# Optimization experiments

Hardware: AMD Instinct MI355X
Metric: run time of the kernel (lower is better)

Reference implementation:

```python
import jax, jax.numpy as jnp
import numpy as np

D_MODEL = 1024
NUM_HEADS = 16
DEPTH = D_MODEL // NUM_HEADS
B, S = 4, 2048


def setup_inputs() -> dict:
    key = jax.random.key(0)
    ks = jax.random.split(key, 13)
    sd = 1.0 / np.sqrt(D_MODEL)
    inp = {
        "q_in": jax.random.normal(ks[0], (B, S, D_MODEL), jnp.float32),
        "k_in": jax.random.normal(ks[1], (B, S, D_MODEL), jnp.float32),
        "v_in": jax.random.normal(ks[2], (B, S, D_MODEL), jnp.float32),
        # binary padding/causal-style mask: 1 = masked position
        "m_in": (jax.random.uniform(ks[3], (B, 1, S, S)) < 0.1).astype(jnp.float32),
        "Wq": jax.random.normal(ks[4], (D_MODEL, D_MODEL), jnp.float32) * sd,
        "bq": jax.random.normal(ks[5], (D_MODEL,), jnp.float32) * 0.01,
        "Wk": jax.random.normal(ks[6], (D_MODEL, D_MODEL), jnp.float32) * sd,
        "bk": jax.random.normal(ks[7], (D_MODEL,), jnp.float32) * 0.01,
        "Wv": jax.random.normal(ks[8], (D_MODEL, D_MODEL), jnp.float32) * sd,
        "bv": jax.random.normal(ks[9], (D_MODEL,), jnp.float32) * 0.01,
        "Wo": jax.random.normal(ks[10], (D_MODEL, D_MODEL), jnp.float32) * sd,
        "bo": jax.random.normal(ks[11], (D_MODEL,), jnp.float32) * 0.01,
    }
    return inp


def _split(t):
    # [B,S,D] -> [B,H,S,depth]
    b, s, _ = t.shape
    return t.reshape(b, s, NUM_HEADS, DEPTH).transpose(0, 2, 1, 3)


def reference(q_in, k_in, v_in, m_in, Wq, bq, Wk, bk, Wv, bv, Wo, bo):
    # torch Linear: x @ W^T + b
    q = _split(q_in @ Wq.T + bq)
    k = _split(k_in @ Wk.T + bk)
    v = _split(v_in @ Wv.T + bv)
    scale = jnp.sqrt(jnp.asarray(DEPTH, jnp.float32))
    scores = jnp.einsum("bhqd,bhkd->bhqk", q, k) / scale
    scores = scores - m_in * 1e6
    attn = jax.nn.softmax(scores, axis=-1)
    out = jnp.einsum("bhqk,bhkd->bhqd", attn, v)  # [B,H,S,depth]
    out = out.transpose(0, 2, 1, 3).reshape(q_in.shape[0], -1, D_MODEL)
    return out @ Wo.T + bo
```

## Files before the change

### kernel.cpp

```cpp
#include <hip/hip_runtime.h>


typedef __bf16 bf16_t;
typedef __bf16 bf16x4 __attribute__((ext_vector_type(4)));
typedef __bf16 bf16x8 __attribute__((ext_vector_type(8)));
typedef float floatx4 __attribute__((ext_vector_type(4)));
typedef float floatx16 __attribute__((ext_vector_type(16)));

#define DMODEL 1024
#define NHEAD  16
#define DEPTH  64
#define BATCH  4
#define SEQ    2048
#define MROWS  (BATCH * SEQ)

#define QSCALE 0.18033688011112042f

#define GLDS16(gaddr, laddr)                                                   \
  __builtin_amdgcn_global_load_lds(                                            \
      (__attribute__((address_space(1))) void*)(gaddr),                        \
      (__attribute__((address_space(3))) void*)(laddr), 16, 0, 0)

__global__ __launch_bounds__(256) void cvt_weights(
    const float* __restrict__ w0, const float* __restrict__ w1,
    const float* __restrict__ w2, const float* __restrict__ w3,
    bf16_t* __restrict__ out) {
  const int n_per4 = (DMODEL * DMODEL) / 4;
  int idx = blockIdx.x * blockDim.x + threadIdx.x;
  int t = idx / n_per4;
  int e4 = idx - t * n_per4;
  const float* src = (t == 0) ? w0 : (t == 1) ? w1 : (t == 2) ? w2 : w3;
  const float sc = (t == 0) ? QSCALE : 1.0f;
  float4 v = ((const float4*)src)[e4];
  bf16_t* dst = out + (size_t)t * (DMODEL * DMODEL) + (size_t)e4 * 4;
  dst[0] = (bf16_t)(v.x * sc); dst[1] = (bf16_t)(v.y * sc);
  dst[2] = (bf16_t)(v.z * sc); dst[3] = (bf16_t)(v.w * sc);
}

__global__ __launch_bounds__(256) void cvt3(
    const float* __restrict__ q, const float* __restrict__ k,
    const float* __restrict__ v, bf16_t* __restrict__ dst) {
  const size_t n8 = (size_t)MROWS * DMODEL / 8;
  size_t i = (size_t)blockIdx.x * blockDim.x + threadIdx.x;
  int t = (int)(i / n8);
  size_t e = i - (size_t)t * n8;
  const float* src = (t == 0) ? q : (t == 1) ? k : v;
  const float4* s = (const float4*)(src + e * 8);
  float4 f0 = s[0], f1 = s[1];
  bf16x8 o;
  o[0] = (bf16_t)f0.x; o[1] = (bf16_t)f0.y; o[2] = (bf16_t)f0.z; o[3] = (bf16_t)f0.w;
  o[4] = (bf16_t)f1.x; o[5] = (bf16_t)f1.y; o[6] = (bf16_t)f1.z; o[7] = (bf16_t)f1.w;
  *(bf16x8*)(dst + i * 8) = o;
}

__global__ __launch_bounds__(256) void mask_prepack(
    const float* __restrict__ m, unsigned int* __restrict__ M32) {
  size_t t = (size_t)blockIdx.x * blockDim.x + threadIdx.x;
  int lane = (int)(t & 63);
  int it = (int)((t >> 6) & 31);
  int g  = (int)((t >> 11) & 63);
  int b  = (int)(t >> 17);
  int q  = g * 32 + (lane & 31);
  int hi = lane >> 5;
  const float* row = m + ((size_t)b * SEQ + q) * SEQ + it * 64;
  unsigned int bits = 0;
#pragma unroll
  for (int kb = 0; kb < 2; kb++) {
#pragma unroll
    for (int rc = 0; rc < 4; rc++) {
      const int base = kb * 32 + 16 * (rc >> 1) + 8 * hi + 4 * (rc & 1);
      const float4 mv = *(const float4*)(row + base);
      const int bit0 = kb * 16 + rc * 4;
      if (mv.x == 0.f) bits |= 1u << (bit0 + 0);
      if (mv.y == 0.f) bits |= 1u << (bit0 + 1);
      if (mv.z == 0.f) bits |= 1u << (bit0 + 2);
      if (mv.w == 0.f) bits |= 1u << (bit0 + 3);
    }
  }
  M32[t] = bits;
}

__global__ __launch_bounds__(256) void gemm_qkv(
    const bf16_t* __restrict__ Abf3, const bf16_t* __restrict__ Wbf,
    const float* __restrict__ bq, const float* __restrict__ bk,
    const float* __restrict__ bv, bf16_t* __restrict__ Qh,
    bf16_t* __restrict__ Kh, bf16_t* __restrict__ Vth) {
  __shared__ __align__(16) bf16_t As[128 * 32];
  __shared__ __align__(16) bf16_t Bs[128 * 32];
  const int K = DMODEL;
  const int tid = threadIdx.x;
  const int lane = tid & 63;
  const int w = tid >> 6;
  const int quad = lane >> 4;
  const int l16 = lane & 15;
  const int wm = w & 1, wn = w >> 1;
  const int z = blockIdx.z;

  const bf16_t* A = Abf3 + (size_t)z * MROWS * DMODEL;
  const bf16_t* Bt = Wbf + (size_t)z * DMODEL * DMODEL;
  const float* bias = (z == 0) ? bq : (z == 1) ? bk : bv;
  const float bias_scale = (z == 0) ? QSCALE : 1.0f;
  bf16_t* Ov = (z == 0) ? Qh : (z == 1) ? Kh : Vth;

  const int lin = blockIdx.x + 8 * blockIdx.y;
  const int c = lin & 7;
  const int j = lin >> 3;
  const int n0 = (j & 7) * 128;
  const int m0 = ((j >> 3) * 8 + c) * 128;

  const int r4 = lane >> 2;
  const int c4 = (lane & 3) ^ (r4 & 3);
  const bf16_t* Ag = A + (size_t)(m0 + w * 32 + r4) * K + c4 * 8;
  const bf16_t* Bg = Bt + (size_t)(n0 + w * 32 + r4) * K + c4 * 8;
  char* AsB = (char*)As + (w * 32) * 64;
  char* BsB = (char*)Bs + (w * 32) * 64;

  floatx4 acc[4][4] = {};

  for (int kk = 0; kk < K; kk += 32) {
    __syncthreads();
    GLDS16(Ag + kk, AsB);
    GLDS16(Ag + kk + (size_t)16 * K, AsB + 16 * 64);
    GLDS16(Bg + kk, BsB);
    GLDS16(Bg + kk + (size_t)16 * K, BsB + 16 * 64);
    __syncthreads();

    bf16x8 af[4], bfr[4];
#pragma unroll
    for (int mi = 0; mi < 4; mi++) {
      const char* Arow = (const char*)As + (wm * 64 + mi * 16 + l16) * 64;
      af[mi] = *(const bf16x8*)(Arow + ((quad ^ (l16 & 3)) * 16));
    }
#pragma unroll
    for (int ni = 0; ni < 4; ni++) {
      const char* Brow = (const char*)Bs + (wn * 64 + ni * 16 + l16) * 64;
      bfr[ni] = *(const bf16x8*)(Brow + ((quad ^ (l16 & 3)) * 16));
    }
#pragma unroll
    for (int mi = 0; mi < 4; mi++)
#pragma unroll
      for (int ni = 0; ni < 4; ni++)
        acc[mi][ni] = __builtin_amdgcn_mfma_f32_16x16x32_bf16(af[mi], bfr[ni], acc[mi][ni], 0, 0, 0);
  }

#pragma unroll
  for (int ni = 0; ni < 4; ni++) {
    const int col = n0 + wn * 64 + ni * 16 + l16;
    const float bvl = bias_scale * bias[col];
    const int hh = col >> 6, d = col & (DEPTH - 1);
#pragma unroll
    for (int mi = 0; mi < 4; mi++) {
#pragma unroll
      for (int r = 0; r < 4; r++) {
        const int row = m0 + wm * 64 + mi * 16 + quad * 4 + r;
        const float val = acc[mi][ni][r] + bvl;
        const int bb = row >> 11, s = row & (SEQ - 1);
        if (z != 2) {
          Ov[((((size_t)bb * NHEAD + hh) * SEQ + s) << 6) + d] = (bf16_t)val;
        } else {
          Ov[(((size_t)bb * NHEAD + hh) * DEPTH + d) * SEQ + s] = (bf16_t)val;
        }
      }
    }
  }
}

__global__ __launch_bounds__(256) void gemm_wo(
    const bf16_t* __restrict__ A, const bf16_t* __restrict__ Bt,
    const float* __restrict__ bias, float* __restrict__ Ov,
    int M, int N, int K) {
  __shared__ __align__(16) bf16_t As[128 * 32];
  __shared__ __align__(16) bf16_t Bs[128 * 32];
  const int tid = threadIdx.x;
  const int lane = tid & 63;
  const int w = tid >> 6;
  const int quad = lane >> 4;
  const int l16 = lane & 15;
  const int wm = w & 1, wn = w >> 1;

  const int lin = blockIdx.x + 8 * blockIdx.y;
  const int c = lin & 7;
  const int j = lin >> 3;
  const int n0 = (j & 7) * 128;
  const int m0 = ((j >> 3) * 8 + c) * 128;

  const int r4 = lane >> 2;
  const int c4 = (lane & 3) ^ (r4 & 3);
  const bf16_t* Ag = A + (size_t)(m0 + w * 32 + r4) * K + c4 * 8;
  const bf16_t* Bg = Bt + (size_t)(n0 + w * 32 + r4) * K + c4 * 8;
  char* AsB = (char*)As + (w * 32) * 64;
  char* BsB = (char*)Bs + (w * 32) * 64;

  floatx4 acc[4][4] = {};

  for (int kk = 0; kk < K; kk += 32) {
    __syncthreads();
    GLDS16(Ag + kk, AsB);
    GLDS16(Ag + kk + (size_t)16 * K, AsB + 16 * 64);
    GLDS16(Bg + kk, BsB);
    GLDS16(Bg + kk + (size_t)16 * K, BsB + 16 * 64);
    __syncthreads();

    bf16x8 af[4], bfr[4];
#pragma unroll
    for (int mi = 0; mi < 4; mi++) {
      const char* Arow = (const char*)As + (wm * 64 + mi * 16 + l16) * 64;
      af[mi] = *(const bf16x8*)(Arow + ((quad ^ (l16 & 3)) * 16));
    }
#pragma unroll
    for (int ni = 0; ni < 4; ni++) {
      const char* Brow = (const char*)Bs + (wn * 64 + ni * 16 + l16) * 64;
      bfr[ni] = *(const bf16x8*)(Brow + ((quad ^ (l16 & 3)) * 16));
    }
#pragma unroll
    for (int mi = 0; mi < 4; mi++)
#pragma unroll
      for (int ni = 0; ni < 4; ni++)
        acc[mi][ni] = __builtin_amdgcn_mfma_f32_16x16x32_bf16(af[mi], bfr[ni], acc[mi][ni], 0, 0, 0);
  }

#pragma unroll
  for (int ni = 0; ni < 4; ni++) {
    const int col = n0 + wn * 64 + ni * 16 + l16;
    const float bv = bias[col];
#pragma unroll
    for (int mi = 0; mi < 4; mi++)
#pragma unroll
      for (int r = 0; r < 4; r++) {
        const int row = m0 + wm * 64 + mi * 16 + quad * 4 + r;
        Ov[(size_t)row * N + col] = acc[mi][ni][r] + bv;
      }
  }
}

__global__ __launch_bounds__(256, 4) void attn_kernel(
    const bf16_t* __restrict__ Qh, const bf16_t* __restrict__ Kh,
    const bf16_t* __restrict__ Vt, const unsigned int* __restrict__ M32,
    bf16_t* __restrict__ O) {
  const int lane = threadIdx.x & 63;
  const int w = __builtin_amdgcn_readfirstlane(threadIdx.x >> 6);
  const int l31 = lane & 31;
  const int hi = lane >> 5;

  const int lin = blockIdx.x + 16 * blockIdx.y + 256 * blockIdx.z;
  const int x8 = lin & 7;
  const int kk = lin >> 3;
  const int qt = kk & 15;
  const int bh = ((kk >> 4) << 3) | x8;
  const int h = bh & 15;
  const int b = bh >> 4;
  const int q0 = qt * 128;

  const bf16_t* Qb = Qh + ((size_t)b * NHEAD + h) * SEQ * DEPTH;
  const bf16_t* Kb = Kh + ((size_t)b * NHEAD + h) * SEQ * DEPTH;
  const bf16_t* Vb = Vt + ((size_t)b * NHEAD + h) * DEPTH * SEQ;
  const unsigned int* Mw =
      M32 + ((size_t)b * 64 + (qt * 4 + w)) * 32 * 64 + lane;

  __shared__ __align__(16) bf16_t Ksm[64 * 64];
  __shared__ __align__(16) bf16_t Vsm[64 * 64];
  __shared__ float Lsm[4][32];

  const int r8 = lane >> 3;
  const int c8 = (lane & 7) ^ r8;
  const int i1 = w * 16 + r8;
  const int i2 = i1 + 8;
  const int lo1 = i1 & 31, lo2 = i2 & 31;
  const int s1 = (i1 & 32) | ((lo1 & ~12) | ((lo1 & 4) << 1) | ((lo1 & 8) >> 1));
  const int s2 = (i2 & 32) | ((lo2 & ~12) | ((lo2 & 4) << 1) | ((lo2 & 8) >> 1));
  const bf16_t* Kg1 = Kb + (size_t)s1 * DEPTH + c8 * 8;
  const bf16_t* Kg2 = Kb + (size_t)s2 * DEPTH + c8 * 8;
  const bf16_t* Vg  = Vb + (size_t)(w * 16 + r8) * SEQ + c8 * 8;
  const int woff = (w * 16) * 128;

  bf16x8 aq[4];
  {
    const bf16_t* qp = Qb + (size_t)(q0 + w * 32 + l31) * DEPTH + hi * 8;
#pragma unroll
    for (int t = 0; t < 4; t++) aq[t] = *(const bf16x8*)(qp + t * 16);
  }

  floatx16 acco[2] = {};
  float lsum = 0.f;
  const int kxor = l31 & 7;

  for (int it = 0; it < SEQ / 64; ++it) {
    const int sk = it * 64;
    __syncthreads();
    {
      char* KsB = (char*)Ksm + woff;
      char* VsB = (char*)Vsm + woff;
      GLDS16(Kg1 + (size_t)sk * DEPTH, KsB);
      GLDS16(Kg2 + (size_t)sk * DEPTH, KsB + 8 * 128);
      GLDS16(Vg + sk, VsB);
      GLDS16(Vg + sk + (size_t)8 * SEQ, VsB + 8 * 128);
    }
    __syncthreads();

    const unsigned int mword = Mw[it * 64];

#pragma unroll
    for (int kb = 0; kb < 2; kb++) {
      floatx16 s = {};
      const char* Krow = (const char*)Ksm + (kb * 32 + l31) * 128;
#pragma unroll
      for (int t = 0; t < 4; t++) {
        bf16x8 kf = *(const bf16x8*)(Krow + (((2 * t + hi) ^ kxor) * 16));
        s = __builtin_amdgcn_mfma_f32_32x32x16_bf16(kf, aq[t], s, 0, 0, 0);
      }
      float pv[16];
#pragma unroll
      for (int r = 0; r < 16; r++) {
        float e = __builtin_amdgcn_exp2f(s[r]);
        const int idx = kb * 16 + r;
        const int km = ((int)(mword << (31 - idx))) >> 31;
        e = __int_as_float(__float_as_int(e) & km);
        lsum += e;
        pv[r] = e;
      }
#pragma unroll
      for (int mh = 0; mh < 2; mh++) {
        bf16x8 pa;
#pragma unroll
        for (int j = 0; j < 8; j++) pa[j] = (bf16_t)pv[mh * 8 + j];
        const int m = kb * 2 + mh;
#pragma unroll
        for (int n = 0; n < 2; n++) {
          const char* Vrow = (const char*)Vsm + (n * 32 + l31) * 128;
          bf16x8 vf = *(const bf16x8*)(Vrow + (((2 * m + hi) ^ kxor) * 16));
          acco[n] = __builtin_amdgcn_mfma_f32_32x32x16_bf16(pa, vf, acco[n], 0, 0, 0);
        }
      }
    }
  }

  float tot = lsum + __shfl_xor(lsum, 32);
  if (lane < 32) Lsm[w][l31] = __frcp_rn(tot);
  __syncthreads();

#pragma unroll
  for (int r = 0; r < 16; r++) {
    const int qr = (r & 3) + 8 * (r >> 2) + 4 * hi;
    const float inv = Lsm[w][qr];
    const size_t srow = (size_t)q0 + w * 32 + qr;
#pragma unroll
    for (int n = 0; n < 2; n++) {
      const int d = h * DEPTH + n * 32 + l31;
      O[((size_t)b * SEQ + srow) * DMODEL + d] = (bf16_t)(acco[n][r] * inv);
    }
  }
}

extern "C" void kernel_launch(void* const* d_in, const int* in_sizes, int n_in,
                              void* d_out, int out_size, void* d_ws, size_t ws_size,
                              hipStream_t stream) {
  const float* q_in = (const float*)d_in[0];
  const float* k_in = (const float*)d_in[1];
  const float* v_in = (const float*)d_in[2];
  const float* m_in = (const float*)d_in[3];
  const float* Wq = (const float*)d_in[4];
  const float* bq = (const float*)d_in[5];
  const float* Wk = (const float*)d_in[6];
  const float* bk = (const float*)d_in[7];
  const float* Wv = (const float*)d_in[8];
  const float* bv = (const float*)d_in[9];
  const float* Wo = (const float*)d_in[10];
  const float* bo = (const float*)d_in[11];

  char* ws = (char*)d_ws;
  const size_t MB = 1024 * 1024;
  bf16_t* wbf  = (bf16_t*)ws;
  bf16_t* Abf3 = (bf16_t*)(ws + 8 * MB);
  bf16_t* Obuf = (bf16_t*)(ws + 8 * MB);
  bf16_t* Qh   = (bf16_t*)(ws + 56 * MB);
  bf16_t* Kh   = (bf16_t*)(ws + 72 * MB);
  bf16_t* Vth  = (bf16_t*)(ws + 88 * MB);
  unsigned int* M32 = (unsigned int*)(ws + 104 * MB);

  cvt_weights<<<(4 * (DMODEL * DMODEL / 4)) / 256, 256, 0, stream>>>(
      Wq, Wk, Wv, Wo, wbf);
  cvt3<<<(3 * (MROWS * DMODEL / 8)) / 256, 256, 0, stream>>>(
      q_in, k_in, v_in, Abf3);
  mask_prepack<<<(BATCH * 64 * 32 * 64) / 256, 256, 0, stream>>>(m_in, M32);

  dim3 gqkv(8, 64, 3);
  gemm_qkv<<<gqkv, 256, 0, stream>>>(Abf3, wbf, bq, bk, bv, Qh, Kh, Vth);

  dim3 ga(SEQ / 128, NHEAD, BATCH);
  attn_kernel<<<ga, 256, 0, stream>>>(Qh, Kh, Vth, M32, Obuf);

  dim3 gg(8, 64);
  gemm_wo<<<gg, 256, 0, stream>>>(
      Obuf, wbf + 3 * (size_t)DMODEL * DMODEL, bo, (float*)d_out,
      MROWS, DMODEL, DMODEL);
}
```

Baseline: 413.0 us.

## Double-buffer LDS in GEMMs and attention, compute row sums via MFMA

Adds two-stage LDS double buffering to the QKV GEMM, the output GEMM and the attention kernel, so the next tile's global-to-LDS load is issued before computing on the current tile, with one barrier per iteration. In attention, the scalar row-sum accumulation and its cross-lane shuffle/LDS reduction are replaced by an extra MFMA against a vector of ones, which yields the per-row sum directly in accumulator layout. It also uses sbfe for mask-bit extraction and s_setprio around MFMA groups. This doubles LDS use per block, which may lower occupancy, and adds MFMA work for the sums.

```diff
diff --git a/kernel.cpp b/kernel.cpp
--- a/kernel.cpp
+++ b/kernel.cpp
@@ -85,8 +85,8 @@
     const float* __restrict__ bq, const float* __restrict__ bk,
     const float* __restrict__ bv, bf16_t* __restrict__ Qh,
     bf16_t* __restrict__ Kh, bf16_t* __restrict__ Vth) {
-  __shared__ __align__(16) bf16_t As[128 * 32];
-  __shared__ __align__(16) bf16_t Bs[128 * 32];
+  __shared__ __align__(16) bf16_t As[2][128 * 32];
+  __shared__ __align__(16) bf16_t Bs[2][128 * 32];
   const int K = DMODEL;
   const int tid = threadIdx.x;
   const int lane = tid & 63;
@@ -112,28 +112,37 @@
   const int c4 = (lane & 3) ^ (r4 & 3);
   const bf16_t* Ag = A + (size_t)(m0 + w * 32 + r4) * K + c4 * 8;
   const bf16_t* Bg = Bt + (size_t)(n0 + w * 32 + r4) * K + c4 * 8;
-  char* AsB = (char*)As + (w * 32) * 64;
-  char* BsB = (char*)Bs + (w * 32) * 64;
+  const int wslice = (w * 32) * 64;
 
   floatx4 acc[4][4] = {};
 
-  for (int kk = 0; kk < K; kk += 32) {
-    __syncthreads();
-    GLDS16(Ag + kk, AsB);
-    GLDS16(Ag + kk + (size_t)16 * K, AsB + 16 * 64);
-    GLDS16(Bg + kk, BsB);
-    GLDS16(Bg + kk + (size_t)16 * K, BsB + 16 * 64);
-    __syncthreads();
+#define STAGEG(kkv, buf)                                                       \
+  do {                                                                         \
+    char* AsB_ = (char*)As[buf] + wslice;                                      \
+    char* BsB_ = (char*)Bs[buf] + wslice;                                      \
+    GLDS16(Ag + (kkv), AsB_);                                                  \
+    GLDS16(Ag + (kkv) + (size_t)16 * K, AsB_ + 16 * 64);                       \
+    GLDS16(Bg + (kkv), BsB_);                                                  \
+    GLDS16(Bg + (kkv) + (size_t)16 * K, BsB_ + 16 * 64);                       \
+  } while (0)
+
+  STAGEG(0, 0);
+  __syncthreads();
+
+  const int NIT = K / 32;
+  for (int t = 0; t < NIT; ++t) {
+    const int cur = t & 1;
+    if (t + 1 < NIT) STAGEG((t + 1) * 32, cur ^ 1);
 
     bf16x8 af[4], bfr[4];
 #pragma unroll
     for (int mi = 0; mi < 4; mi++) {
-      const char* Arow = (const char*)As + (wm * 64 + mi * 16 + l16) * 64;
+      const char* Arow = (const char*)As[cur] + (wm * 64 + mi * 16 + l16) * 64;
       af[mi] = *(const bf16x8*)(Arow + ((quad ^ (l16 & 3)) * 16));
     }
 #pragma unroll
     for (int ni = 0; ni < 4; ni++) {
-      const char* Brow = (const char*)Bs + (wn * 64 + ni * 16 + l16) * 64;
+      const char* Brow = (const char*)Bs[cur] + (wn * 64 + ni * 16 + l16) * 64;
       bfr[ni] = *(const bf16x8*)(Brow + ((quad ^ (l16 & 3)) * 16));
     }
 #pragma unroll
@@ -141,7 +150,9 @@
 #pragma unroll
       for (int ni = 0; ni < 4; ni++)
         acc[mi][ni] = __builtin_amdgcn_mfma_f32_16x16x32_bf16(af[mi], bfr[ni], acc[mi][ni], 0, 0, 0);
-  }
+    __syncthreads();
+  }
+#undef STAGEG
 
 #pragma unroll
   for (int ni = 0; ni < 4; ni++) {
@@ -169,8 +180,8 @@
     const bf16_t* __restrict__ A, const bf16_t* __restrict__ Bt,
     const float* __restrict__ bias, float* __restrict__ Ov,
     int M, int N, int K) {
-  __shared__ __align__(16) bf16_t As[128 * 32];
-  __shared__ __align__(16) bf16_t Bs[128 * 32];
+  __shared__ __align__(16) bf16_t As[2][128 * 32];
+  __shared__ __align__(16) bf16_t Bs[2][128 * 32];
   const int tid = threadIdx.x;
   const int lane = tid & 63;
   const int w = tid >> 6;
@@ -188,28 +199,37 @@
   const int c4 = (lane & 3) ^ (r4 & 3);
   const bf16_t* Ag = A + (size_t)(m0 + w * 32 + r4) * K + c4 * 8;
   const bf16_t* Bg = Bt + (size_t)(n0 + w * 32 + r4) * K + c4 * 8;
-  char* AsB = (char*)As + (w * 32) * 64;
-  char* BsB = (char*)Bs + (w * 32) * 64;
+  const int wslice = (w * 32) * 64;
 
   floatx4 acc[4][4] = {};
 
-  for (int kk = 0; kk < K; kk += 32) {
-    __syncthreads();
-    GLDS16(Ag + kk, AsB);
-    GLDS16(Ag + kk + (size_t)16 * K, AsB + 16 * 64);
-    GLDS16(Bg + kk, BsB);
-    GLDS16(Bg + kk + (size_t)16 * K, BsB + 16 * 64);
-    __syncthreads();
+#define STAGEG(kkv, buf)                                                       \
+  do {                                                                         \
+    char* AsB_ = (char*)As[buf] + wslice;                                      \
+    char* BsB_ = (char*)Bs[buf] + wslice;                                      \
+    GLDS16(Ag + (kkv), AsB_);                                                  \
+    GLDS16(Ag + (kkv) + (size_t)16 * K, AsB_ + 16 * 64);                       \
+    GLDS16(Bg + (kkv), BsB_);                                                  \
+    GLDS16(Bg + (kkv) + (size_t)16 * K, BsB_ + 16 * 64);                       \
+  } while (0)
+
+  STAGEG(0, 0);
+  __syncthreads();
+
+  const int NIT = K / 32;
+  for (int t = 0; t < NIT; ++t) {
+    const int cur = t & 1;
+    if (t + 1 < NIT) STAGEG((t + 1) * 32, cur ^ 1);
 
     bf16x8 af[4], bfr[4];
 #pragma unroll
     for (int mi = 0; mi < 4; mi++) {
-      const char* Arow = (const char*)As + (wm * 64 + mi * 16 + l16) * 64;
+      const char* Arow = (const char*)As[cur] + (wm * 64 + mi * 16 + l16) * 64;
       af[mi] = *(const bf16x8*)(Arow + ((quad ^ (l16 & 3)) * 16));
     }
 #pragma unroll
     for (int ni = 0; ni < 4; ni++) {
-      const char* Brow = (const char*)Bs + (wn * 64 + ni * 16 + l16) * 64;
+      const char* Brow = (const char*)Bs[cur] + (wn * 64 + ni * 16 + l16) * 64;
       bfr[ni] = *(const bf16x8*)(Brow + ((quad ^ (l16 & 3)) * 16));
     }
 #pragma unroll
@@ -217,7 +237,9 @@
 #pragma unroll
       for (int ni = 0; ni < 4; ni++)
         acc[mi][ni] = __builtin_amdgcn_mfma_f32_16x16x32_bf16(af[mi], bfr[ni], acc[mi][ni], 0, 0, 0);
-  }
+    __syncthreads();
+  }
+#undef STAGEG
 
 #pragma unroll
   for (int ni = 0; ni < 4; ni++) {
@@ -257,9 +279,8 @@
   const unsigned int* Mw =
       M32 + ((size_t)b * 64 + (qt * 4 + w)) * 32 * 64 + lane;
 
-  __shared__ __align__(16) bf16_t Ksm[64 * 64];
-  __shared__ __align__(16) bf16_t Vsm[64 * 64];
-  __shared__ float Lsm[4][32];
+  __shared__ __align__(16) bf16_t Ksm[2][64 * 64];
+  __shared__ __align__(16) bf16_t Vsm[2][64 * 64];
 
   const int r8 = lane >> 3;
   const int c8 = (lane & 7) ^ r8;
@@ -280,68 +301,80 @@
     for (int t = 0; t < 4; t++) aq[t] = *(const bf16x8*)(qp + t * 16);
   }
 
+  bf16x8 vone;
+#pragma unroll
+  for (int j2 = 0; j2 < 8; j2++) vone[j2] = (bf16_t)1.0f;
+
   floatx16 acco[2] = {};
-  float lsum = 0.f;
+  floatx16 accl = {};
   const int kxor = l31 & 7;
 
-  for (int it = 0; it < SEQ / 64; ++it) {
-    const int sk = it * 64;
-    __syncthreads();
-    {
-      char* KsB = (char*)Ksm + woff;
-      char* VsB = (char*)Vsm + woff;
-      GLDS16(Kg1 + (size_t)sk * DEPTH, KsB);
-      GLDS16(Kg2 + (size_t)sk * DEPTH, KsB + 8 * 128);
-      GLDS16(Vg + sk, VsB);
-      GLDS16(Vg + sk + (size_t)8 * SEQ, VsB + 8 * 128);
-    }
-    __syncthreads();
+#define STAGE(itv, buf)                                                        \
+  do {                                                                         \
+    const int sk_ = (itv) * 64;                                                \
+    char* KsB_ = (char*)Ksm[buf] + woff;                                       \
+    char* VsB_ = (char*)Vsm[buf] + woff;                                       \
+    GLDS16(Kg1 + (size_t)sk_ * DEPTH, KsB_);                                   \
+    GLDS16(Kg2 + (size_t)sk_ * DEPTH, KsB_ + 8 * 128);                         \
+    GLDS16(Vg + sk_, VsB_);                                                    \
+    GLDS16(Vg + sk_ + (size_t)8 * SEQ, VsB_ + 8 * 128);                        \
+  } while (0)
+
+  STAGE(0, 0);
+  __syncthreads();
+
+  const int NT = SEQ / 64;
+  for (int it = 0; it < NT; ++it) {
+    const int cur = it & 1;
+    if (it + 1 < NT) STAGE(it + 1, cur ^ 1);
 
     const unsigned int mword = Mw[it * 64];
+    const char* Kbuf = (const char*)Ksm[cur];
+    const char* Vbuf = (const char*)Vsm[cur];
 
 #pragma unroll
     for (int kb = 0; kb < 2; kb++) {
       floatx16 s = {};
-      const char* Krow = (const char*)Ksm + (kb * 32 + l31) * 128;
+      const char* Krow = Kbuf + (kb * 32 + l31) * 128;
+      __builtin_amdgcn_s_setprio(1);
 #pragma unroll
       for (int t = 0; t < 4; t++) {
         bf16x8 kf = *(const bf16x8*)(Krow + (((2 * t + hi) ^ kxor) * 16));
         s = __builtin_amdgcn_mfma_f32_32x32x16_bf16(kf, aq[t], s, 0, 0, 0);
       }
+      __builtin_amdgcn_s_setprio(0);
       float pv[16];
 #pragma unroll
       for (int r = 0; r < 16; r++) {
         float e = __builtin_amdgcn_exp2f(s[r]);
-        const int idx = kb * 16 + r;
-        const int km = ((int)(mword << (31 - idx))) >> 31;
-        e = __int_as_float(__float_as_int(e) & km);
-        lsum += e;
-        pv[r] = e;
+        const int km = __builtin_amdgcn_sbfe((int)mword, kb * 16 + r, 1);
+        pv[r] = __int_as_float(__float_as_int(e) & km);
       }
 #pragma unroll
       for (int mh = 0; mh < 2; mh++) {
         bf16x8 pa;
 #pragma unroll
-        for (int j = 0; j < 8; j++) pa[j] = (bf16_t)pv[mh * 8 + j];
+        for (int j2 = 0; j2 < 8; j2++) pa[j2] = (bf16_t)pv[mh * 8 + j2];
         const int m = kb * 2 + mh;
+        __builtin_amdgcn_s_setprio(1);
+        accl = __builtin_amdgcn_mfma_f32_32x32x16_bf16(pa, vone, accl, 0, 0, 0);
 #pragma unroll
         for (int n = 0; n < 2; n++) {
-          const char* Vrow = (const char*)Vsm + (n * 32 + l31) * 128;
+          const char* Vrow = Vbuf + (n * 32 + l31) * 128;
           bf16x8 vf = *(const bf16x8*)(Vrow + (((2 * m + hi) ^ kxor) * 16));
           acco[n] = __builtin_amdgcn_mfma_f32_32x32x16_bf16(pa, vf, acco[n], 0, 0, 0);
         }
+        __builtin_amdgcn_s_setprio(0);
       }
     }
-  }
-
-  float tot = lsum + __shfl_xor(lsum, 32);
-  if (lane < 32) Lsm[w][l31] = __frcp_rn(tot);
-  __syncthreads();
+    __syncthreads();
+  }
+#undef STAGE
 
 #pragma unroll
   for (int r = 0; r < 16; r++) {
+    const float inv = __frcp_rn(accl[r]);
     const int qr = (r & 3) + 8 * (r >> 2) + 4 * hi;
-    const float inv = Lsm[w][qr];
     const size_t srow = (size_t)q0 + w * 32 + qr;
 #pragma unroll
     for (int n = 0; n < 2; n++) {
```

Result: slower. 422.6 us (+2.3%).

## Double GEMM K-tile to 64 and tighten attention softmax inner loop

Applied to the files above, without the earlier changes.

Both projection GEMMs now stage 64-wide K slices per iteration with an 8-way XOR swizzle, which halves the number of barrier pairs and loop iterations. In attention, the mask bit is extracted with a single bitfield-extract instruction, and the row sum is accumulated as a two-lane float vector so packed adds can be used and the serial add chain is split. The mask word load is also moved ahead of the barrier. The cost is double the shared memory per GEMM block, which may reduce occupancy, and a changed summation order.

```diff
diff --git a/kernel.cpp b/kernel.cpp
--- a/kernel.cpp
+++ b/kernel.cpp
@@ -4,6 +4,7 @@
 typedef __bf16 bf16_t;
 typedef __bf16 bf16x4 __attribute__((ext_vector_type(4)));
 typedef __bf16 bf16x8 __attribute__((ext_vector_type(8)));
+typedef float floatx2 __attribute__((ext_vector_type(2)));
 typedef float floatx4 __attribute__((ext_vector_type(4)));
 typedef float floatx16 __attribute__((ext_vector_type(16)));
 
@@ -85,8 +86,8 @@
     const float* __restrict__ bq, const float* __restrict__ bk,
     const float* __restrict__ bv, bf16_t* __restrict__ Qh,
     bf16_t* __restrict__ Kh, bf16_t* __restrict__ Vth) {
-  __shared__ __align__(16) bf16_t As[128 * 32];
-  __shared__ __align__(16) bf16_t Bs[128 * 32];
+  __shared__ __align__(16) bf16_t As[128 * 64];
+  __shared__ __align__(16) bf16_t Bs[128 * 64];
   const int K = DMODEL;
   const int tid = threadIdx.x;
   const int lane = tid & 63;
@@ -108,39 +109,43 @@
   const int n0 = (j & 7) * 128;
   const int m0 = ((j >> 3) * 8 + c) * 128;
 
-  const int r4 = lane >> 2;
-  const int c4 = (lane & 3) ^ (r4 & 3);
-  const bf16_t* Ag = A + (size_t)(m0 + w * 32 + r4) * K + c4 * 8;
-  const bf16_t* Bg = Bt + (size_t)(n0 + w * 32 + r4) * K + c4 * 8;
-  char* AsB = (char*)As + (w * 32) * 64;
-  char* BsB = (char*)Bs + (w * 32) * 64;
+  const int r8l = lane >> 3;
+  const int c8l = (lane & 7) ^ r8l;
+  const bf16_t* Ag = A + (size_t)(m0 + w * 32 + r8l) * K + c8l * 8;
+  const bf16_t* Bg = Bt + (size_t)(n0 + w * 32 + r8l) * K + c8l * 8;
+  char* AsB = (char*)As + (w * 32) * 128;
+  char* BsB = (char*)Bs + (w * 32) * 128;
 
   floatx4 acc[4][4] = {};
 
-  for (int kk = 0; kk < K; kk += 32) {
-    __syncthreads();
-    GLDS16(Ag + kk, AsB);
-    GLDS16(Ag + kk + (size_t)16 * K, AsB + 16 * 64);
-    GLDS16(Bg + kk, BsB);
-    GLDS16(Bg + kk + (size_t)16 * K, BsB + 16 * 64);
-    __syncthreads();
-
-    bf16x8 af[4], bfr[4];
-#pragma unroll
-    for (int mi = 0; mi < 4; mi++) {
-      const char* Arow = (const char*)As + (wm * 64 + mi * 16 + l16) * 64;
-      af[mi] = *(const bf16x8*)(Arow + ((quad ^ (l16 & 3)) * 16));
-    }
-#pragma unroll
-    for (int ni = 0; ni < 4; ni++) {
-      const char* Brow = (const char*)Bs + (wn * 64 + ni * 16 + l16) * 64;
-      bfr[ni] = *(const bf16x8*)(Brow + ((quad ^ (l16 & 3)) * 16));
-    }
-#pragma unroll
-    for (int mi = 0; mi < 4; mi++)
-#pragma unroll
-      for (int ni = 0; ni < 4; ni++)
-        acc[mi][ni] = __builtin_amdgcn_mfma_f32_16x16x32_bf16(af[mi], bfr[ni], acc[mi][ni], 0, 0, 0);
+  for (int kk = 0; kk < K; kk += 64) {
+    __syncthreads();
+#pragma unroll
+    for (int cl = 0; cl < 4; cl++) {
+      GLDS16(Ag + kk + (size_t)(cl * 8) * K, AsB + cl * 8 * 128);
+      GLDS16(Bg + kk + (size_t)(cl * 8) * K, BsB + cl * 8 * 128);
+    }
+    __syncthreads();
+
+#pragma unroll
+    for (int kk2 = 0; kk2 < 2; kk2++) {
+      bf16x8 af[4], bfr[4];
+#pragma unroll
+      for (int mi = 0; mi < 4; mi++) {
+        const char* Arow = (const char*)As + (wm * 64 + mi * 16 + l16) * 128;
+        af[mi] = *(const bf16x8*)(Arow + (((kk2 * 4 + quad) ^ (l16 & 7)) * 16));
+      }
+#pragma unroll
+      for (int ni = 0; ni < 4; ni++) {
+        const char* Brow = (const char*)Bs + (wn * 64 + ni * 16 + l16) * 128;
+        bfr[ni] = *(const bf16x8*)(Brow + (((kk2 * 4 + quad) ^ (l16 & 7)) * 16));
+      }
+#pragma unroll
+      for (int mi = 0; mi < 4; mi++)
+#pragma unroll
+        for (int ni = 0; ni < 4; ni++)
+          acc[mi][ni] = __builtin_amdgcn_mfma_f32_16x16x32_bf16(af[mi], bfr[ni], acc[mi][ni], 0, 0, 0);
+    }
   }
 
 #pragma unroll
@@ -169,8 +174,8 @@
     const bf16_t* __restrict__ A, const bf16_t* __restrict__ Bt,
     const float* __restrict__ bias, float* __restrict__ Ov,
     int M, int N, int K) {
-  __shared__ __align__(16) bf16_t As[128 * 32];
-  __shared__ __align__(16) bf16_t Bs[128 * 32];
+  __shared__ __align__(16) bf16_t As[128 * 64];
+  __shared__ __align__(16) bf16_t Bs[128 * 64];
   const int tid = threadIdx.x;
   const int lane = tid & 63;
   const int w = tid >> 6;
@@ -184,39 +189,43 @@
   const int n0 = (j & 7) * 128;
   const int m0 = ((j >> 3) * 8 + c) * 128;
 
-  const int r4 = lane >> 2;
-  const int c4 = (lane & 3) ^ (r4 & 3);
-  const bf16_t* Ag = A + (size_t)(m0 + w * 32 + r4) * K + c4 * 8;
-  const bf16_t* Bg = Bt + (size_t)(n0 + w * 32 + r4) * K + c4 * 8;
-  char* AsB = (char*)As + (w * 32) * 64;
-  char* BsB = (char*)Bs + (w * 32) * 64;
+  const int r8l = lane >> 3;
+  const int c8l = (lane & 7) ^ r8l;
+  const bf16_t* Ag = A + (size_t)(m0 + w * 32 + r8l) * K + c8l * 8;
+  const bf16_t* Bg = Bt + (size_t)(n0 + w * 32 + r8l) * K + c8l * 8;
+  char* AsB = (char*)As + (w * 32) * 128;
+  char* BsB = (char*)Bs + (w * 32) * 128;
 
   floatx4 acc[4][4] = {};
 
-  for (int kk = 0; kk < K; kk += 32) {
-    __syncthreads();
-    GLDS16(Ag + kk, AsB);
-    GLDS16(Ag + kk + (size_t)16 * K, AsB + 16 * 64);
-    GLDS16(Bg + kk, BsB);
-    GLDS16(Bg + kk + (size_t)16 * K, BsB + 16 * 64);
-    __syncthreads();
-
-    bf16x8 af[4], bfr[4];
-#pragma unroll
-    for (int mi = 0; mi < 4; mi++) {
-      const char* Arow = (const char*)As + (wm * 64 + mi * 16 + l16) * 64;
-      af[mi] = *(const bf16x8*)(Arow + ((quad ^ (l16 & 3)) * 16));
-    }
-#pragma unroll
-    for (int ni = 0; ni < 4; ni++) {
-      const char* Brow = (const char*)Bs + (wn * 64 + ni * 16 + l16) * 64;
-      bfr[ni] = *(const bf16x8*)(Brow + ((quad ^ (l16 & 3)) * 16));
-    }
-#pragma unroll
-    for (int mi = 0; mi < 4; mi++)
-#pragma unroll
-      for (int ni = 0; ni < 4; ni++)
-        acc[mi][ni] = __builtin_amdgcn_mfma_f32_16x16x32_bf16(af[mi], bfr[ni], acc[mi][ni], 0, 0, 0);
+  for (int kk = 0; kk < K; kk += 64) {
+    __syncthreads();
+#pragma unroll
+    for (int cl = 0; cl < 4; cl++) {
+      GLDS16(Ag + kk + (size_t)(cl * 8) * K, AsB + cl * 8 * 128);
+      GLDS16(Bg + kk + (size_t)(cl * 8) * K, BsB + cl * 8 * 128);
+    }
+    __syncthreads();
+
+#pragma unroll
+    for (int kk2 = 0; kk2 < 2; kk2++) {
+      bf16x8 af[4], bfr[4];
+#pragma unroll
+      for (int mi = 0; mi < 4; mi++) {
+        const char* Arow = (const char*)As + (wm * 64 + mi * 16 + l16) * 128;
+        af[mi] = *(const bf16x8*)(Arow + (((kk2 * 4 + quad) ^ (l16 & 7)) * 16));
+      }
+#pragma unroll
+      for (int ni = 0; ni < 4; ni++) {
+        const char* Brow = (const char*)Bs + (wn * 64 + ni * 16 + l16) * 128;
+        bfr[ni] = *(const bf16x8*)(Brow + (((kk2 * 4 + quad) ^ (l16 & 7)) * 16));
+      }
+#pragma unroll
+      for (int mi = 0; mi < 4; mi++)
+#pragma unroll
+        for (int ni = 0; ni < 4; ni++)
+          acc[mi][ni] = __builtin_amdgcn_mfma_f32_16x16x32_bf16(af[mi], bfr[ni], acc[mi][ni], 0, 0, 0);
+    }
   }
 
 #pragma unroll
@@ -281,11 +290,12 @@
   }
 
   floatx16 acco[2] = {};
-  float lsum = 0.f;
+  floatx2 l2 = {0.f, 0.f};
   const int kxor = l31 & 7;
 
   for (int it = 0; it < SEQ / 64; ++it) {
     const int sk = it * 64;
+    const unsigned int mword = Mw[it * 64];
     __syncthreads();
     {
       char* KsB = (char*)Ksm + woff;
@@ -297,8 +307,6 @@
     }
     __syncthreads();
 
-    const unsigned int mword = Mw[it * 64];
-
 #pragma unroll
     for (int kb = 0; kb < 2; kb++) {
       floatx16 s = {};
@@ -312,17 +320,17 @@
 #pragma unroll
       for (int r = 0; r < 16; r++) {
         float e = __builtin_amdgcn_exp2f(s[r]);
-        const int idx = kb * 16 + r;
-        const int km = ((int)(mword << (31 - idx))) >> 31;
-        e = __int_as_float(__float_as_int(e) & km);
-        lsum += e;
-        pv[r] = e;
-      }
+        const int km = __builtin_amdgcn_sbfe((int)mword, kb * 16 + r, 1);
+        pv[r] = __int_as_float(__float_as_int(e) & km);
+      }
+#pragma unroll
+      for (int r = 0; r < 8; r++)
+        l2 += (floatx2){pv[2 * r], pv[2 * r + 1]};
 #pragma unroll
       for (int mh = 0; mh < 2; mh++) {
         bf16x8 pa;
 #pragma unroll
-        for (int j = 0; j < 8; j++) pa[j] = (bf16_t)pv[mh * 8 + j];
+        for (int j2 = 0; j2 < 8; j2++) pa[j2] = (bf16_t)pv[mh * 8 + j2];
         const int m = kb * 2 + mh;
 #pragma unroll
         for (int n = 0; n < 2; n++) {
@@ -334,6 +342,7 @@
     }
   }
 
+  float lsum = l2.x + l2.y;
   float tot = lsum + __shfl_xor(lsum, 32);
   if (lane < 32) Lsm[w][l31] = __frcp_rn(tot);
   __syncthreads();
```

After: 405.3 us. No clear change (-1.9%).
